# Kernel optimization log

Measured on AMD Instinct MI355X. Metric: run time of the kernel, lower is better.

## Reference

```python
import jax, jax.numpy as jnp
import numpy as np

N, B, F = 204800, 4096, 256

def setup_inputs() -> dict:
    key = jax.random.key(0)
    ks = jax.random.split(key, 8)
    s = 1.0 / np.sqrt(F)
    return {
        'node_feats': jax.random.normal(ks[0], (N, F), jnp.float32),
        'g_feats': jax.random.normal(ks[1], (B, F), jnp.float32),
        'segment_ids': jnp.sort(jax.random.randint(ks[2], (N,), 0, B, jnp.int32)),
        'W_logit': jax.random.normal(ks[3], (1, 2 * F), jnp.float32) * (1.0 / np.sqrt(2 * F)),
        'b_logit': jnp.zeros((1,), jnp.float32),
        'W_proj': jax.random.normal(ks[4], (F, F), jnp.float32) * s,
        'b_proj': jnp.zeros((F,), jnp.float32),
        'W_ih': jax.random.normal(ks[5], (3 * F, F), jnp.float32) * s,
        'W_hh': jax.random.normal(ks[6], (3 * F, F), jnp.float32) * s,
        'b_ih': jnp.zeros((3 * F,), jnp.float32),
        'b_hh': jnp.zeros((3 * F,), jnp.float32),
    }

def reference(node_feats, g_feats, segment_ids, W_logit, b_logit, W_proj, b_proj, W_ih, W_hh, b_ih, b_hh):
    num_graphs = g_feats.shape[0]
    # logits: Linear(2F -> 1) on [broadcast(relu(g_feats)), node_feats], then LeakyReLU(0.01)
    ctx_nodes = jax.nn.relu(g_feats)[segment_ids]                      # [N, F]
    z = jnp.concatenate([ctx_nodes, node_feats], axis=1) @ W_logit.T + b_logit  # [N, 1]
    z = jax.nn.leaky_relu(z, negative_slope=0.01)
    # per-graph segment softmax over nodes
    zmax = jax.ops.segment_max(z, segment_ids, num_segments=num_graphs)
    z_exp = jnp.exp(z - zmax[segment_ids])
    denom = jax.ops.segment_sum(z_exp, segment_ids, num_segments=num_graphs)
    a = z_exp / denom[segment_ids]                                     # [N, 1]
    # project nodes (Dropout is identity at eval) and weighted segment sum
    hv = node_feats @ W_proj.T + b_proj                                # [N, F]
    g_repr = jax.ops.segment_sum(a * hv, segment_ids, num_segments=num_graphs)  # [B, F]
    context = jax.nn.elu(g_repr)
    # PyTorch GRUCell: input=context, hidden=g_feats
    gi = context @ W_ih.T + b_ih                                       # [B, 3F]
    gh = g_feats @ W_hh.T + b_hh
    i_r, i_z, i_n = jnp.split(gi, 3, axis=1)
    h_r, h_z, h_n = jnp.split(gh, 3, axis=1)
    r = jax.nn.sigmoid(i_r + h_r)
    zg = jax.nn.sigmoid(i_z + h_z)
    n = jnp.tanh(i_n + r * h_n)
    return (1.0 - zg) * n + zg * g_feats
```

## Files before the change

kernel.cpp:

```cpp
#include <hip/hip_runtime.h>

#define NN 204800
#define BB 4096
#define FF 256
#define CAP 72

typedef unsigned short u16;
typedef unsigned int u32;
typedef short bf16x8 __attribute__((ext_vector_type(8)));
typedef float f32x4  __attribute__((ext_vector_type(4)));
typedef float f4     __attribute__((ext_vector_type(4)));

__device__ __forceinline__ u16 rne_bf16(float f){
    union { u32 v; float f; } t; t.f = f;
    u32 lsb = (t.v >> 16) & 1u;
    t.v += 0x7fffu + lsb;
    return (u16)(t.v >> 16);
}
__device__ __forceinline__ float bf16_to_f(u16 h){
    union { u32 v; float f; } t; t.v = (u32)h << 16; return t.f;
}
__device__ __forceinline__ void cvt4(const float* __restrict__ src, u16* __restrict__ dst){
    float4 v = *(const float4*)src;
    ushort4 h;
    h.x = rne_bf16(v.x); h.y = rne_bf16(v.y);
    h.z = rne_bf16(v.z); h.w = rne_bf16(v.w);
    *(ushort4*)dst = h;
}

__global__ void k_prep(const float* __restrict__ gfe, const float* __restrict__ Wp,
                       const float* __restrict__ Wih, const float* __restrict__ Whh,
                       const int* __restrict__ seg, int* __restrict__ start,
                       u16* __restrict__ gfe_b, u16* __restrict__ Wp_b,
                       u16* __restrict__ Wih_b, u16* __restrict__ Whh_b){
    int i = blockIdx.x * 256 + threadIdx.x;
    if (i <= BB){
        int lo = 0, hi = NN;
        while (lo < hi){ int mid = (lo + hi) >> 1; if (seg[mid] < i) lo = mid + 1; else hi = mid; }
        start[i] = lo;
    }
    const int n_gfe = BB * FF;
    const int n_wp  = FF * FF;
    const int n_w3  = 3 * FF * FF;
    int j = i * 4;
    if (j < n_gfe){ cvt4(gfe + j, gfe_b + j); return; }
    j -= n_gfe;
    if (j < n_wp){ cvt4(Wp + j, Wp_b + j); return; }
    j -= n_wp;
    if (j < n_w3){ cvt4(Wih + j, Wih_b + j); return; }
    j -= n_w3;
    if (j < n_w3){ cvt4(Whh + j, Whh_b + j); return; }
}
#define PREP_V4 ((BB*FF + FF*FF + 2*3*FF*FF) / 4)

__global__ __launch_bounds__(256) void k_attn(
        const float* __restrict__ x, const float* __restrict__ Wl,
        const float* __restrict__ bl, const float* __restrict__ gfe,
        const int* __restrict__ start, u16* __restrict__ s_b){
    __shared__ __align__(16) u16 xs[CAP][FF];
    __shared__ float zs[512];
    __shared__ float red[16];
    int g = blockIdx.x;
    int s0 = start[g], cnt = start[g + 1] - s0;
    int tid = threadIdx.x, wave = tid >> 6, lane = tid & 63;
    if (cnt == 0){
        s_b[(size_t)g * FF + tid] = 0;
        return;
    }
    float p = Wl[tid] * fmaxf(gfe[(size_t)g * FF + tid], 0.f);
    #pragma unroll
    for (int o = 32; o; o >>= 1) p += __shfl_xor(p, o);
    if (lane == 0) red[8 + wave] = p;
    float blv = bl[0];
    f4 wv = *(const f4*)(Wl + FF + lane * 4);

    auto st_row = [&](int row, const f4& v){
        ushort4 h;
        h.x = rne_bf16(v.x); h.y = rne_bf16(v.y);
        h.z = rne_bf16(v.z); h.w = rne_bf16(v.w);
        *(ushort4*)(&xs[row][lane * 4]) = h;
    };

    int i = wave;
    for (; i + 12 < cnt; i += 16){
        const f4* r0 = (const f4*)(x + (size_t)(s0 + i) * FF + lane * 4);
        f4 xv0 = __builtin_nontemporal_load(r0);
        f4 xv1 = __builtin_nontemporal_load(r0 + FF);
        f4 xv2 = __builtin_nontemporal_load(r0 + 2 * FF);
        f4 xv3 = __builtin_nontemporal_load(r0 + 3 * FF);
        float d0 = xv0.x * wv.x + xv0.y * wv.y + xv0.z * wv.z + xv0.w * wv.w;
        float d1 = xv1.x * wv.x + xv1.y * wv.y + xv1.z * wv.z + xv1.w * wv.w;
        float d2 = xv2.x * wv.x + xv2.y * wv.y + xv2.z * wv.z + xv2.w * wv.w;
        float d3 = xv3.x * wv.x + xv3.y * wv.y + xv3.z * wv.z + xv3.w * wv.w;
        #pragma unroll
        for (int o = 32; o; o >>= 1){
            d0 += __shfl_xor(d0, o); d1 += __shfl_xor(d1, o);
            d2 += __shfl_xor(d2, o); d3 += __shfl_xor(d3, o);
        }
        if (i      < CAP) st_row(i,      xv0);
        if (i + 4  < CAP) st_row(i + 4,  xv1);
        if (i + 8  < CAP) st_row(i + 8,  xv2);
        if (i + 12 < CAP) st_row(i + 12, xv3);
        if (lane == 0){
            zs[i] = d0; zs[i + 4] = d1; zs[i + 8] = d2; zs[i + 12] = d3;
        }
    }
    for (; i < cnt; i += 4){
        f4 xv = *(const f4*)(x + (size_t)(s0 + i) * FF + lane * 4);
        float d = xv.x * wv.x + xv.y * wv.y + xv.z * wv.z + xv.w * wv.w;
        #pragma unroll
        for (int o = 32; o; o >>= 1) d += __shfl_xor(d, o);
        if (i < CAP) st_row(i, xv);
        if (lane == 0) zs[i] = d;
    }
    __syncthreads();
    float cg = red[8] + red[9] + red[10] + red[11] + blv;
    float mx = -3.4e38f;
    for (int k = tid; k < cnt; k += 256){
        float t = cg + zs[k];
        t = t >= 0.f ? t : 0.01f * t;
        zs[k] = t;
        mx = fmaxf(mx, t);
    }
    #pragma unroll
    for (int o = 32; o; o >>= 1) mx = fmaxf(mx, __shfl_xor(mx, o));
    if (lane == 0) red[wave] = mx;
    __syncthreads();
    mx = fmaxf(fmaxf(red[0], red[1]), fmaxf(red[2], red[3]));
    float dsum = 0.f;
    for (int k = tid; k < cnt; k += 256){
        float e = expf(zs[k] - mx);
        zs[k] = e;
        dsum += e;
    }
    #pragma unroll
    for (int o = 32; o; o >>= 1) dsum += __shfl_xor(dsum, o);
    if (lane == 0) red[4 + wave] = dsum;
    __syncthreads();
    float inv = 1.f / (red[4] + red[5] + red[6] + red[7]);
    float acc = 0.f;
    int lim = cnt < CAP ? cnt : CAP;
    for (int k = 0; k < lim; k++) acc += zs[k] * bf16_to_f(xs[k][tid]);
    for (int k = CAP; k < cnt; k++) acc += zs[k] * x[(size_t)(s0 + k) * FF + tid];
    s_b[(size_t)g * FF + tid] = rne_bf16(acc * inv);
}

#define CPAD 264
__global__ __launch_bounds__(512) void k_proj_gru(
        const u16* __restrict__ s_b, const u16* __restrict__ Wp_b,
        const float* __restrict__ bp, const int* __restrict__ start,
        const u16* __restrict__ gfe_b, const u16* __restrict__ Wih_b,
        const u16* __restrict__ Whh_b, const float* __restrict__ bih,
        const float* __restrict__ bhh, const float* __restrict__ gfe,
        float* __restrict__ out){
    __shared__ __align__(16) u16 ctx_s[16][CPAD];
    int tid = threadIdx.x;
    int w = tid >> 6, l = tid & 63;
    int mn = l & 15, q = l >> 4;
    int g0 = blockIdx.x * 16;
    int fb = w * 32;
    f32x4 acc[2] = {};
    const u16* arow = s_b + (size_t)(g0 + mn) * FF + q * 8;
    #pragma unroll
    for (int kb = 0; kb < 8; kb++){
        bf16x8 a = *(const bf16x8*)(arow + kb * 32);
        #pragma unroll
        for (int cc = 0; cc < 2; cc++){
            bf16x8 b = *(const bf16x8*)(Wp_b + (size_t)(fb + cc * 16 + mn) * FF + kb * 32 + q * 8);
            acc[cc] = __builtin_amdgcn_mfma_f32_16x16x32_bf16(a, b, acc[cc], 0, 0, 0);
        }
    }
    #pragma unroll
    for (int cc = 0; cc < 2; cc++){
        int f = fb + cc * 16 + mn;
        float bias = bp[f];
        #pragma unroll
        for (int r = 0; r < 4; r++){
            int g = g0 + q * 4 + r;
            float bs = (start[g + 1] > start[g]) ? 1.f : 0.f;
            float v = acc[cc][r] + bs * bias;
            v = v > 0.f ? v : expm1f(v);
            ctx_s[q * 4 + r][f] = rne_bf16(v);
        }
    }
    __syncthreads();
    f32x4 ai[3][2] = {};
    f32x4 ah[3][2] = {};
    const u16* ag_row = gfe_b + (size_t)(g0 + mn) * FF + q * 8;
    #pragma unroll
    for (int kb = 0; kb < 8; kb++){
        bf16x8 a_c = *(const bf16x8*)(&ctx_s[mn][kb * 32 + q * 8]);
        bf16x8 a_g = *(const bf16x8*)(ag_row + kb * 32);
        #pragma unroll
        for (int s = 0; s < 3; s++){
            #pragma unroll
            for (int cc = 0; cc < 2; cc++){
                size_t woff = (size_t)(s * FF + fb + cc * 16 + mn) * FF + kb * 32 + q * 8;
                bf16x8 bi = *(const bf16x8*)(Wih_b + woff);
                ai[s][cc] = __builtin_amdgcn_mfma_f32_16x16x32_bf16(a_c, bi, ai[s][cc], 0, 0, 0);
                bf16x8 bh = *(const bf16x8*)(Whh_b + woff);
                ah[s][cc] = __builtin_amdgcn_mfma_f32_16x16x32_bf16(a_g, bh, ah[s][cc], 0, 0, 0);
            }
        }
    }
    #pragma unroll
    for (int cc = 0; cc < 2; cc++){
        int f = fb + cc * 16 + mn;
        float bir = bih[f], biz = bih[FF + f], bin_ = bih[2 * FF + f];
        float bhr = bhh[f], bhz = bhh[FF + f], bhn = bhh[2 * FF + f];
        #pragma unroll
        for (int r = 0; r < 4; r++){
            int g = g0 + q * 4 + r;
            float rg = 1.f / (1.f + expf(-(ai[0][cc][r] + bir + ah[0][cc][r] + bhr)));
            float zg = 1.f / (1.f + expf(-(ai[1][cc][r] + biz + ah[1][cc][r] + bhz)));
            float ng = tanhf(ai[2][cc][r] + bin_ + rg * (ah[2][cc][r] + bhn));
            float h = gfe[(size_t)g * FF + f];
            out[(size_t)g * FF + f] = (1.f - zg) * ng + zg * h;
        }
    }
}

extern "C" void kernel_launch(void* const* d_in, const int* in_sizes, int n_in,
                              void* d_out, int out_size, void* d_ws, size_t ws_size,
                              hipStream_t stream){
    const float* node = (const float*)d_in[0];
    const float* gfe  = (const float*)d_in[1];
    const int*   seg  = (const int*)d_in[2];
    const float* Wl   = (const float*)d_in[3];
    const float* bl   = (const float*)d_in[4];
    const float* Wp   = (const float*)d_in[5];
    const float* bp   = (const float*)d_in[6];
    const float* Wih  = (const float*)d_in[7];
    const float* Whh  = (const float*)d_in[8];
    const float* bih  = (const float*)d_in[9];
    const float* bhh  = (const float*)d_in[10];
    float* out = (float*)d_out;

    char* p = (char*)d_ws;
    auto alloc = [&](size_t bytes)->void*{
        void* r = (void*)p; p += (bytes + 255) & ~(size_t)255; return r;
    };
    int*   start = (int*)  alloc((BB + 1) * sizeof(int));
    u16*   s_b   = (u16*)  alloc((size_t)BB * FF * sizeof(u16));
    u16*   gfe_b = (u16*)  alloc((size_t)BB * FF * sizeof(u16));
    u16*   Wp_b  = (u16*)  alloc((size_t)FF * FF * sizeof(u16));
    u16*   Wih_b = (u16*)  alloc((size_t)3 * FF * FF * sizeof(u16));
    u16*   Whh_b = (u16*)  alloc((size_t)3 * FF * FF * sizeof(u16));

    k_prep<<<(PREP_V4 + 255) / 256, 256, 0, stream>>>(gfe, Wp, Wih, Whh, seg, start,
                                                      gfe_b, Wp_b, Wih_b, Whh_b);
    k_attn<<<BB, 256, 0, stream>>>(node, Wl, bl, gfe, start, s_b);
    k_proj_gru<<<BB / 16, 512, 0, stream>>>(s_b, Wp_b, bp, start, gfe_b, Wih_b, Whh_b,
                                            bih, bhh, gfe, out);
}
```

Before: 343.8 us.

## Fold prep kernel into attention kernel with wave-parallel segment search

Removes the separate prep launch. Its work moves into the attention kernel: each block converts its own graph-feature row and a slice of the weights to bf16, and finds its segment bounds with a 64-way ballot-based search. A per-graph gate flag replaces the start array in the GRU kernel. The node streaming loop is also widened to 8 rows per wave per iteration, which adds memory-level parallelism at the cost of more registers. The intent is to cut a kernel launch and its serialization, accepting extra per-block prologue latency.

```diff
diff --git a/kernel.cpp b/kernel.cpp
--- a/kernel.cpp
+++ b/kernel.cpp
@@ -28,51 +28,70 @@
     *(ushort4*)dst = h;
 }
 
-__global__ void k_prep(const float* __restrict__ gfe, const float* __restrict__ Wp,
-                       const float* __restrict__ Wih, const float* __restrict__ Whh,
-                       const int* __restrict__ seg, int* __restrict__ start,
-                       u16* __restrict__ gfe_b, u16* __restrict__ Wp_b,
-                       u16* __restrict__ Wih_b, u16* __restrict__ Whh_b){
-    int i = blockIdx.x * 256 + threadIdx.x;
-    if (i <= BB){
-        int lo = 0, hi = NN;
-        while (lo < hi){ int mid = (lo + hi) >> 1; if (seg[mid] < i) lo = mid + 1; else hi = mid; }
-        start[i] = lo;
-    }
-    const int n_gfe = BB * FF;
-    const int n_wp  = FF * FF;
-    const int n_w3  = 3 * FF * FF;
-    int j = i * 4;
-    if (j < n_gfe){ cvt4(gfe + j, gfe_b + j); return; }
-    j -= n_gfe;
-    if (j < n_wp){ cvt4(Wp + j, Wp_b + j); return; }
-    j -= n_wp;
-    if (j < n_w3){ cvt4(Wih + j, Wih_b + j); return; }
-    j -= n_w3;
-    if (j < n_w3){ cvt4(Whh + j, Whh_b + j); return; }
-}
-#define PREP_V4 ((BB*FF + FF*FF + 2*3*FF*FF) / 4)
+__device__ __forceinline__ int lb64(const int* __restrict__ seg, int val, int lane){
+    int lo = 0, hi = NN;
+    while (lo < hi){
+        int span = (hi - lo + 63) >> 6;
+        int pos = lo + lane * span;
+        int v = (pos < hi) ? seg[pos] : 0x7fffffff;
+        unsigned long long m = __ballot(v < val);
+        if (m == 0ull){ hi = lo; break; }
+        int h = 63 - __clzll(m);
+        int nlo = lo + h * span + 1;
+        int nhi = lo + (h + 1) * span;
+        lo = nlo;
+        hi = nhi < hi ? nhi : hi;
+    }
+    return lo;
+}
+
+#define CVT_V4 ((FF*FF + 2*3*FF*FF) / 4)
 
 __global__ __launch_bounds__(256) void k_attn(
         const float* __restrict__ x, const float* __restrict__ Wl,
         const float* __restrict__ bl, const float* __restrict__ gfe,
-        const int* __restrict__ start, u16* __restrict__ s_b){
+        const int* __restrict__ seg, u16* __restrict__ s_b,
+        u16* __restrict__ gfe_b, float* __restrict__ gate,
+        const float* __restrict__ Wp, const float* __restrict__ Wih,
+        const float* __restrict__ Whh, u16* __restrict__ Wp_b,
+        u16* __restrict__ Wih_b, u16* __restrict__ Whh_b){
     __shared__ __align__(16) u16 xs[CAP][FF];
     __shared__ float zs[512];
     __shared__ float red[16];
+    __shared__ int sbounds[2];
     int g = blockIdx.x;
-    int s0 = start[g], cnt = start[g + 1] - s0;
     int tid = threadIdx.x, wave = tid >> 6, lane = tid & 63;
+
+    float gv = gfe[(size_t)g * FF + tid];
+    gfe_b[(size_t)g * FF + tid] = rne_bf16(gv);
+    float p = Wl[tid] * fmaxf(gv, 0.f);
+    #pragma unroll
+    for (int o = 32; o; o >>= 1) p += __shfl_xor(p, o);
+    if (lane == 0) red[8 + wave] = p;
+
+    int gid = g * 256 + tid;
+    if (gid < CVT_V4){
+        int j = gid * 4;
+        const int n_wp = FF * FF, n_w3 = 3 * FF * FF;
+        if (j < n_wp)            cvt4(Wp + j, Wp_b + j);
+        else if ((j -= n_wp) < n_w3) cvt4(Wih + j, Wih_b + j);
+        else                     cvt4(Whh + (j - n_w3), Whh_b + (j - n_w3));
+    }
+
+    if (wave < 2){
+        int L = lb64(seg, g + wave, lane);
+        if (lane == 0) sbounds[wave] = L;
+    }
+    float blv = bl[0];
+    f4 wv = *(const f4*)(Wl + FF + lane * 4);
+    __syncthreads();
+
+    int s0 = sbounds[0], cnt = sbounds[1] - s0;
+    if (tid == 0) gate[g] = cnt > 0 ? 1.f : 0.f;
     if (cnt == 0){
         s_b[(size_t)g * FF + tid] = 0;
         return;
     }
-    float p = Wl[tid] * fmaxf(gfe[(size_t)g * FF + tid], 0.f);
-    #pragma unroll
-    for (int o = 32; o; o >>= 1) p += __shfl_xor(p, o);
-    if (lane == 0) red[8 + wave] = p;
-    float blv = bl[0];
-    f4 wv = *(const f4*)(Wl + FF + lane * 4);
 
     auto st_row = [&](int row, const f4& v){
         ushort4 h;
@@ -82,31 +101,50 @@
     };
 
     int i = wave;
+    for (; i + 28 < cnt; i += 32){
+        const f4* r0 = (const f4*)(x + (size_t)(s0 + i) * FF + lane * 4);
+        f4 xv[8];
+        #pragma unroll
+        for (int u = 0; u < 8; u++) xv[u] = __builtin_nontemporal_load(r0 + u * FF);
+        float d[8];
+        #pragma unroll
+        for (int u = 0; u < 8; u++)
+            d[u] = xv[u].x * wv.x + xv[u].y * wv.y + xv[u].z * wv.z + xv[u].w * wv.w;
+        #pragma unroll
+        for (int o = 32; o; o >>= 1){
+            #pragma unroll
+            for (int u = 0; u < 8; u++) d[u] += __shfl_xor(d[u], o);
+        }
+        #pragma unroll
+        for (int u = 0; u < 8; u++) if (i + u * 4 < CAP) st_row(i + u * 4, xv[u]);
+        if (lane == 0){
+            #pragma unroll
+            for (int u = 0; u < 8; u++) zs[i + u * 4] = d[u];
+        }
+    }
     for (; i + 12 < cnt; i += 16){
         const f4* r0 = (const f4*)(x + (size_t)(s0 + i) * FF + lane * 4);
-        f4 xv0 = __builtin_nontemporal_load(r0);
-        f4 xv1 = __builtin_nontemporal_load(r0 + FF);
-        f4 xv2 = __builtin_nontemporal_load(r0 + 2 * FF);
-        f4 xv3 = __builtin_nontemporal_load(r0 + 3 * FF);
-        float d0 = xv0.x * wv.x + xv0.y * wv.y + xv0.z * wv.z + xv0.w * wv.w;
-        float d1 = xv1.x * wv.x + xv1.y * wv.y + xv1.z * wv.z + xv1.w * wv.w;
-        float d2 = xv2.x * wv.x + xv2.y * wv.y + xv2.z * wv.z + xv2.w * wv.w;
-        float d3 = xv3.x * wv.x + xv3.y * wv.y + xv3.z * wv.z + xv3.w * wv.w;
+        f4 xv[4];
+        #pragma unroll
+        for (int u = 0; u < 4; u++) xv[u] = __builtin_nontemporal_load(r0 + u * FF);
+        float d[4];
+        #pragma unroll
+        for (int u = 0; u < 4; u++)
+            d[u] = xv[u].x * wv.x + xv[u].y * wv.y + xv[u].z * wv.z + xv[u].w * wv.w;
         #pragma unroll
         for (int o = 32; o; o >>= 1){
-            d0 += __shfl_xor(d0, o); d1 += __shfl_xor(d1, o);
-            d2 += __shfl_xor(d2, o); d3 += __shfl_xor(d3, o);
-        }
-        if (i      < CAP) st_row(i,      xv0);
-        if (i + 4  < CAP) st_row(i + 4,  xv1);
-        if (i + 8  < CAP) st_row(i + 8,  xv2);
-        if (i + 12 < CAP) st_row(i + 12, xv3);
+            #pragma unroll
+            for (int u = 0; u < 4; u++) d[u] += __shfl_xor(d[u], o);
+        }
+        #pragma unroll
+        for (int u = 0; u < 4; u++) if (i + u * 4 < CAP) st_row(i + u * 4, xv[u]);
         if (lane == 0){
-            zs[i] = d0; zs[i + 4] = d1; zs[i + 8] = d2; zs[i + 12] = d3;
+            #pragma unroll
+            for (int u = 0; u < 4; u++) zs[i + u * 4] = d[u];
         }
     }
     for (; i < cnt; i += 4){
-        f4 xv = *(const f4*)(x + (size_t)(s0 + i) * FF + lane * 4);
+        f4 xv = __builtin_nontemporal_load((const f4*)(x + (size_t)(s0 + i) * FF + lane * 4));
         float d = xv.x * wv.x + xv.y * wv.y + xv.z * wv.z + xv.w * wv.w;
         #pragma unroll
         for (int o = 32; o; o >>= 1) d += __shfl_xor(d, o);
@@ -148,7 +186,7 @@
 #define CPAD 264
 __global__ __launch_bounds__(512) void k_proj_gru(
         const u16* __restrict__ s_b, const u16* __restrict__ Wp_b,
-        const float* __restrict__ bp, const int* __restrict__ start,
+        const float* __restrict__ bp, const float* __restrict__ gate,
         const u16* __restrict__ gfe_b, const u16* __restrict__ Wih_b,
         const u16* __restrict__ Whh_b, const float* __restrict__ bih,
         const float* __restrict__ bhh, const float* __restrict__ gfe,
@@ -177,8 +215,7 @@
         #pragma unroll
         for (int r = 0; r < 4; r++){
             int g = g0 + q * 4 + r;
-            float bs = (start[g + 1] > start[g]) ? 1.f : 0.f;
-            float v = acc[cc][r] + bs * bias;
+            float v = acc[cc][r] + gate[g] * bias;
             v = v > 0.f ? v : expm1f(v);
             ctx_s[q * 4 + r][f] = rne_bf16(v);
         }
@@ -240,16 +277,15 @@
     auto alloc = [&](size_t bytes)->void*{
         void* r = (void*)p; p += (bytes + 255) & ~(size_t)255; return r;
     };
-    int*   start = (int*)  alloc((BB + 1) * sizeof(int));
+    float* gate  = (float*)alloc(BB * sizeof(float));
     u16*   s_b   = (u16*)  alloc((size_t)BB * FF * sizeof(u16));
     u16*   gfe_b = (u16*)  alloc((size_t)BB * FF * sizeof(u16));
     u16*   Wp_b  = (u16*)  alloc((size_t)FF * FF * sizeof(u16));
     u16*   Wih_b = (u16*)  alloc((size_t)3 * FF * FF * sizeof(u16));
     u16*   Whh_b = (u16*)  alloc((size_t)3 * FF * FF * sizeof(u16));
 
-    k_prep<<<(PREP_V4 + 255) / 256, 256, 0, stream>>>(gfe, Wp, Wih, Whh, seg, start,
-                                                      gfe_b, Wp_b, Wih_b, Whh_b);
-    k_attn<<<BB, 256, 0, stream>>>(node, Wl, bl, gfe, start, s_b);
-    k_proj_gru<<<BB / 16, 512, 0, stream>>>(s_b, Wp_b, bp, start, gfe_b, Wih_b, Whh_b,
+    k_attn<<<BB, 256, 0, stream>>>(node, Wl, bl, gfe, seg, s_b, gfe_b, gate,
+                                   Wp, Wih, Whh, Wp_b, Wih_b, Whh_b);
+    k_proj_gru<<<BB / 16, 512, 0, stream>>>(s_b, Wp_b, bp, gate, gfe_b, Wih_b, Whh_b,
                                             bih, bhh, gfe, out);
 }
```

Measured after the change: 337.3 us. No clear change (-1.9%).
